# Performance work log

Measured on AMD Instinct MI355X. Metric: run time of the kernel, lower is better.

The kernel has to match this reference:

```python
import jax, jax.numpy as jnp
import numpy as np

T_IN, T_OUT, B, D, H, L = 257, 256, 256, 131, 256, 2


def lstm_cell(x, h, c, Wih, Whh, bih, bhh):
    # torch LSTMCell gate order: i, f, g, o
    z = x @ Wih.T + h @ Whh.T + bih + bhh
    i, f, g, o = jnp.split(z, 4, axis=-1)
    c_new = jax.nn.sigmoid(f) * c + jax.nn.sigmoid(i) * jnp.tanh(g)
    h_new = jax.nn.sigmoid(o) * jnp.tanh(c_new)
    return h_new, c_new


def setup_inputs() -> dict:
    key = jax.random.key(0)
    ks = jax.random.split(key, 22)
    s = 0.05  # weight scale, keeps gates in the linear-ish region
    d = {}
    d["X"] = jax.random.normal(ks[0], (T_IN, B, D), jnp.float32)
    d["Y"] = jax.random.normal(ks[1], (T_OUT, B, D), jnp.float32)
    shapes = {
        "enc_Wih0": (4 * H, D), "enc_Whh0": (4 * H, H), "enc_bih0": (4 * H,), "enc_bhh0": (4 * H,),
        "enc_Wih1": (4 * H, H), "enc_Whh1": (4 * H, H), "enc_bih1": (4 * H,), "enc_bhh1": (4 * H,),
        "dec_Wih0": (4 * H, D), "dec_Whh0": (4 * H, H), "dec_bih0": (4 * H,), "dec_bhh0": (4 * H,),
        "dec_Wih1": (4 * H, H), "dec_Whh1": (4 * H, H), "dec_bih1": (4 * H,), "dec_bhh1": (4 * H,),
        "lin_W": (D, H), "lin_b": (D,),
    }
    for i, (name, shp) in enumerate(shapes.items()):
        d[name] = jax.random.normal(ks[2 + i], shp, jnp.float32) * s
    return d


def _make_step(params, emit):
    def step(carry, x):
        hs, cs = carry
        inp = x
        new_h, new_c = [], []
        for l, (Wih, Whh, bih, bhh) in enumerate(params):
            h, c = lstm_cell(inp, hs[l], cs[l], Wih, Whh, bih, bhh)
            new_h.append(h)
            new_c.append(c)
            inp = h
        out = emit(inp) if emit is not None else None
        return (tuple(new_h), tuple(new_c)), out
    return step


def reference(X, Y, enc_Wih0, enc_Whh0, enc_bih0, enc_bhh0,
              enc_Wih1, enc_Whh1, enc_bih1, enc_bhh1,
              dec_Wih0, dec_Whh0, dec_bih0, dec_bhh0,
              dec_Wih1, dec_Whh1, dec_bih1, dec_bhh1,
              lin_W, lin_b):
    enc = [(enc_Wih0, enc_Whh0, enc_bih0, enc_bhh0),
           (enc_Wih1, enc_Whh1, enc_bih1, enc_bhh1)]
    dec = [(dec_Wih0, dec_Whh0, dec_bih0, dec_bhh0),
           (dec_Wih1, dec_Whh1, dec_bih1, dec_bhh1)]
    b = X.shape[1]
    zeros = tuple(jnp.zeros((b, H), X.dtype) for _ in range(L))
    # encoder over X[:-1]
    (hn, cn), _ = jax.lax.scan(_make_step(enc, None), (zeros, zeros), X[:-1])
    # decoder (teacher forcing): inputs are [X[-1], Y[0], ..., Y[T_out-2]]
    dec_in = jnp.concatenate([X[-1:], Y[:-1]], axis=0)
    emit = lambda h: jax.nn.log_softmax(h @ lin_W.T + lin_b, axis=-1)
    _, Ypred = jax.lax.scan(_make_step(dec, emit), (hn, cn), dec_in)
    return Ypred  # (T_out, B, out_dim) log-probabilities
```

## Files before the change

kernel.cpp:

```cpp
#include <hip/hip_runtime.h>
#include <hip/hip_bf16.h>
#include <math.h>

typedef __attribute__((ext_vector_type(8))) short short8;
typedef __attribute__((ext_vector_type(4))) float f32x4;
typedef unsigned long long u64;

#define STEPS 512
#define BB 256
#define HH 256
#define DD 131
#define XP 160
#define K0P 416
#define KS0 424
#define K1  512
#define KS1 520
#define HS0 264
#define HS1 520
#define RING 16
#define PO   8
#define NGRP 8
#define ROWS 32
#define SLOT_E (ROWS * HH)
#define RGELEM (RING * SLOT_E)
#define POISON64 0x7F807F807F807F80ull

#define OFF_W0E 0
#define OFF_W0D (OFF_W0E + 1024 * K0P)
#define OFF_W1E (OFF_W0D + 1024 * K0P)
#define OFF_W1D (OFF_W1E + 1024 * K1)
#define OFF_LW  (OFF_W1D + 1024 * K1)
#define OFF_XBF (OFF_LW + 160 * 256)
#define OFF_H0R (OFF_XBF + (size_t)STEPS * BB * XP)
#define OFF_H1R (OFF_H0R + (size_t)NGRP * RGELEM)
#define OFF_H1A (OFF_H1R + (size_t)NGRP * RGELEM)
#define OFF_BF16_END (OFF_H1A + (size_t)256 * BB * HH)

#define LDS_W_OFF  0
#define LDS_HS_OFF 66560
#define LDS_TOTAL  133120

__device__ __forceinline__ float rcp_(float x) { return __builtin_amdgcn_rcpf(x); }
__device__ __forceinline__ float fsigm(float x) { return rcp_(1.f + __expf(-x)); }
__device__ __forceinline__ float ftanh(float x) {
    float t = __expf(-2.f * fabsf(x));
    float r = (1.f - t) * rcp_(1.f + t);
    return copysignf(r, x);
}
__device__ __forceinline__ u64 aload(const u64* p) {
    return __hip_atomic_load(p, __ATOMIC_RELAXED, __HIP_MEMORY_SCOPE_AGENT);
}
__device__ __forceinline__ void astore(u64* p, u64 v) {
    __hip_atomic_store(p, v, __ATOMIC_RELAXED, __HIP_MEMORY_SCOPE_AGENT);
}

__global__ __launch_bounds__(256) void pack_w0(const float* __restrict__ Wih,
                                               const float* __restrict__ Whh,
                                               __hip_bfloat16* __restrict__ dst) {
    int idx = blockIdx.x * 256 + threadIdx.x;
    int p = idx / K0P, k = idx - p * K0P;
    int ct = p >> 6, local = p & 63, g = local >> 4, j = local & 15;
    int orow = g * 256 + ct * 16 + j;
    float v = 0.f;
    if (k < DD) v = Wih[orow * DD + k];
    else if (k >= XP) v = Whh[orow * HH + (k - XP)];
    dst[idx] = __float2bfloat16(v);
}

__global__ __launch_bounds__(256) void pack_w1(const float* __restrict__ Wih,
                                               const float* __restrict__ Whh,
                                               __hip_bfloat16* __restrict__ dst) {
    int idx = blockIdx.x * 256 + threadIdx.x;
    int p = idx >> 9, k = idx & 511;
    int ct = p >> 6, local = p & 63, g = local >> 4, j = local & 15;
    int orow = g * 256 + ct * 16 + j;
    float v = (k < HH) ? Wih[orow * HH + k] : Whh[orow * HH + (k - HH)];
    dst[idx] = __float2bfloat16(v);
}

__global__ __launch_bounds__(256) void pack_bias(const float* __restrict__ bih,
                                                 const float* __restrict__ bhh,
                                                 float* __restrict__ dst) {
    int idx = blockIdx.x * 256 + threadIdx.x;
    if (idx < 1024) dst[idx] = bih[idx] + bhh[idx];
}

__global__ __launch_bounds__(256) void pack_xbf(const float* __restrict__ X,
                                                const float* __restrict__ Y,
                                                __hip_bfloat16* __restrict__ dst) {
    int idx = blockIdx.x * 256 + threadIdx.x;
    int kp = idx % XP;
    int rb = idx / XP;
    int b = rb & 255, s = rb >> 8;
    const float* src;
    if (s <= 256) src = X + ((size_t)s * BB + b) * DD;
    else          src = Y + ((size_t)(s - 257) * BB + b) * DD;
    dst[idx] = __float2bfloat16(kp < DD ? src[kp] : 0.f);
}

__global__ __launch_bounds__(256) void pack_linw(const float* __restrict__ linW,
                                                 __hip_bfloat16* __restrict__ dst) {
    int idx = blockIdx.x * 256 + threadIdx.x;
    int j = idx >> 8, k = idx & 255;
    dst[idx] = __float2bfloat16(j < DD ? linW[j * HH + k] : 0.f);
}

__global__ __launch_bounds__(256) void pack_linb(const float* __restrict__ linb,
                                                 float* __restrict__ dst) {
    int idx = threadIdx.x;
    if (idx < 160) dst[idx] = (idx < DD) ? linb[idx] : -1.0e30f;
}

__global__ __launch_bounds__(256) void init_rings(u64* __restrict__ rings,
                                                  int* __restrict__ acks) {
    int idx = blockIdx.x * 256 + threadIdx.x;
    if (idx < 2 * NGRP * (RGELEM / 4)) {
        int slot = (idx >> 11) & (RING - 1);
        rings[idx] = (slot == RING - 1) ? 0ull : POISON64;
    }
    if (idx < 256) acks[idx] = 0;
}

__global__ __launch_bounds__(512, 1) void lstm_persistent(
    const __hip_bfloat16* __restrict__ wsb,
    const float* __restrict__ bsum,
    __hip_bfloat16* __restrict__ h0ring,
    __hip_bfloat16* __restrict__ h1ring,
    __hip_bfloat16* __restrict__ h1all,
    int* __restrict__ acks) {
    extern __shared__ __align__(16) char lds[];
    __hip_bfloat16* Wlds = (__hip_bfloat16*)(lds + LDS_W_OFF);
    __hip_bfloat16* hst  = (__hip_bfloat16*)(lds + LDS_HS_OFF);

    const int tid = threadIdx.x;
    const int wg = blockIdx.x;
    const int xg = wg >> 5;
    const int slot_id = wg & 31;
    const int layer = slot_id >> 4;
    const int ct = slot_id & 15;
    const int lane = tid & 63;
    const int mt = tid >> 6;
    const int lrow = lane & 15;
    const int lk8 = (lane >> 4) * 8;

    const int K  = layer ? K1 : K0P;
    const int KS = layer ? KS1 : KS0;
    const int HS = layer ? HS1 : HS0;
    int* ackp = acks + xg * 32;

    auto load_w = [&](int ph2) {
        const __hip_bfloat16* src = wsb +
            (layer ? (ph2 ? OFF_W1D : OFF_W1E) : (ph2 ? OFF_W0D : OFF_W0E)) +
            (size_t)ct * 64 * K;
        const int KC = K >> 3;
        for (int e = tid; e < 64 * KC; e += 512) {
            int p = e / KC, kc = e - p * KC;
            *(short8*)&Wlds[p * KS + kc * 8] =
                *(const short8*)&src[(size_t)p * K + kc * 8];
        }
    };
    load_w(0);

    const int jcol = ct * 16 + lrow;
    float br[2][4];
    #pragma unroll
    for (int ph = 0; ph < 2; ++ph)
        #pragma unroll
        for (int g = 0; g < 4; ++g)
            br[ph][g] = bsum[ph * 2048 + layer * 1024 + g * 256 + jcol];
    f32x4 creg = {0.f, 0.f, 0.f, 0.f};

    const __hip_bfloat16* Xbf = wsb + OFF_XBF;
    __hip_bfloat16* h0g = h0ring + (size_t)xg * RGELEM;
    __hip_bfloat16* h1g = h1ring + (size_t)xg * RGELEM;
    __hip_bfloat16* ringw = layer ? h1g : h0g;
    const int arow = mt * 16 + lrow;
    __syncthreads();

    for (int s = 0; s < STEPS; ++s) {
        const int ph = s >> 8;
        const bool defer_x = (s == 256);
        f32x4 acc[4];
        short8 xv[5];

        if (tid < 128) {
            #pragma unroll
            for (int g = 0; g < 4; ++g) acc[g] = (f32x4){0.f, 0.f, 0.f, 0.f};
            if (layer == 0) {
                const short8* xp = (const short8*)
                    &Xbf[((size_t)s * BB + xg * ROWS + arow) * XP];
                #pragma unroll
                for (int kt = 0; kt < 5; ++kt) xv[kt] = xp[kt * 4 + (lk8 >> 3)];
                if (!defer_x) {
                    #pragma unroll
                    for (int kt = 0; kt < 5; ++kt)
                        #pragma unroll
                        for (int g = 0; g < 4; ++g) {
                            short8 w = *(const short8*)
                                &Wlds[(g * 16 + lrow) * KS0 + kt * 32 + lk8];
                            acc[g] = __builtin_amdgcn_mfma_f32_16x16x32_bf16(
                                xv[kt], w, acc[g], 0, 0, 0);
                        }
                }
            }
        } else {
            const int ptid = tid - 128;
            __hip_bfloat16* hs = hst + (s & 1) * 32 * HS;
            if (layer == 0) {
                const u64* src = (const u64*)(h0g +
                    (size_t)((s + RING - 1) & (RING - 1)) * SLOT_E);
                u64 v[6];
                unsigned pend = 0;
                #pragma unroll
                for (int i = 0; i < 6; ++i)
                    if (ptid + i * 384 < 2048) pend |= (1u << i);
                int guard = 0;
                while (pend) {
                    #pragma unroll
                    for (int i = 0; i < 6; ++i)
                        if (pend & (1u << i)) v[i] = aload(src + ptid + i * 384);
                    unsigned np = 0;
                    #pragma unroll
                    for (int i = 0; i < 6; ++i)
                        if ((pend & (1u << i)) &&
                            ((v[i] & 0xFFFFull) == 0x7F80ull)) np |= (1u << i);
                    pend = np;
                    if (pend) {
                        __builtin_amdgcn_s_sleep(1);
                        if (++guard > 65536) break;
                    }
                }
                #pragma unroll
                for (int i = 0; i < 6; ++i) {
                    int p = ptid + i * 384;
                    if (p < 2048) {
                        int row = p >> 6, c = p & 63;
                        *(u64*)&hs[row * HS0 + c * 4] = v[i];
                    }
                }
                if (ptid == 383) {
                    int tgt = 16 * (s - (PO - 1));
                    if (tgt > 0) {
                        int guard2 = 0;
                        while (__hip_atomic_load(ackp, __ATOMIC_RELAXED,
                                                 __HIP_MEMORY_SCOPE_AGENT) < tgt) {
                            __builtin_amdgcn_s_sleep(1);
                            if (++guard2 > 65536) break;
                        }
                    }
                }
            } else {
                const u64* s0 = (const u64*)(h0g +
                    (size_t)(s & (RING - 1)) * SLOT_E);
                const u64* s1 = (const u64*)(h1g +
                    (size_t)((s + RING - 1) & (RING - 1)) * SLOT_E);
                u64 v[11];
                unsigned pend = 0;
                #pragma unroll
                for (int i = 0; i < 11; ++i)
                    if (ptid + i * 384 < 4096) pend |= (1u << i);
                int guard = 0;
                while (pend) {
                    #pragma unroll
                    for (int i = 0; i < 11; ++i)
                        if (pend & (1u << i)) {
                            int p = ptid + i * 384;
                            v[i] = aload(p < 2048 ? s0 + p : s1 + (p - 2048));
                        }
                    unsigned np = 0;
                    #pragma unroll
                    for (int i = 0; i < 11; ++i)
                        if ((pend & (1u << i)) &&
                            ((v[i] & 0xFFFFull) == 0x7F80ull)) np |= (1u << i);
                    pend = np;
                    if (pend) {
                        __builtin_amdgcn_s_sleep(1);
                        if (++guard > 65536) break;
                    }
                }
                #pragma unroll
                for (int i = 0; i < 11; ++i) {
                    int p = ptid + i * 384;
                    if (p < 4096) {
                        int pr = p & 2047;
                        int row = pr >> 6, c = pr & 63;
                        *(u64*)&hs[row * HS1 + (p < 2048 ? 0 : 256) + c * 4] = v[i];
                    }
                }
            }
        }
        __syncthreads();
        if (s == 256) { load_w(1); __syncthreads(); }

        if (tid < 128) {
            if (layer == 1 && tid == 0)
                __hip_atomic_fetch_add(ackp, 1, __ATOMIC_RELAXED,
                                       __HIP_MEMORY_SCOPE_AGENT);
            const __hip_bfloat16* hs = hst + (s & 1) * 32 * HS;
            if (layer == 0) {
                if (defer_x) {
                    #pragma unroll
                    for (int kt = 0; kt < 5; ++kt)
                        #pragma unroll
                        for (int g = 0; g < 4; ++g) {
                            short8 w = *(const short8*)
                                &Wlds[(g * 16 + lrow) * KS0 + kt * 32 + lk8];
                            acc[g] = __builtin_amdgcn_mfma_f32_16x16x32_bf16(
                                xv[kt], w, acc[g], 0, 0, 0);
                        }
                }
                #pragma unroll
                for (int kt = 0; kt < 8; ++kt) {
                    short8 a = *(const short8*)&hs[arow * HS0 + kt * 32 + lk8];
                    #pragma unroll
                    for (int g = 0; g < 4; ++g) {
                        short8 w = *(const short8*)
                            &Wlds[(g * 16 + lrow) * KS0 + (5 + kt) * 32 + lk8];
                        acc[g] = __builtin_amdgcn_mfma_f32_16x16x32_bf16(
                            a, w, acc[g], 0, 0, 0);
                    }
                }
            } else {
                #pragma unroll
                for (int kt = 0; kt < 16; ++kt) {
                    short8 a = *(const short8*)&hs[arow * HS1 + kt * 32 + lk8];
                    #pragma unroll
                    for (int g = 0; g < 4; ++g) {
                        short8 w = *(const short8*)
                            &Wlds[(g * 16 + lrow) * KS1 + kt * 32 + lk8];
                        acc[g] = __builtin_amdgcn_mfma_f32_16x16x32_bf16(
                            a, w, acc[g], 0, 0, 0);
                    }
                }
            }

            unsigned short hu[4];
            #pragma unroll
            for (int r = 0; r < 4; ++r) {
                float zi = acc[0][r] + br[ph][0];
                float zf = acc[1][r] + br[ph][1];
                float zg = acc[2][r] + br[ph][2];
                float zo = acc[3][r] + br[ph][3];
                float ig = fsigm(zi), fg = fsigm(zf), og = fsigm(zo);
                float cn = fg * creg[r] + ig * ftanh(zg);
                creg[r] = cn;
                union { __hip_bfloat16 b; unsigned short u; } cvt;
                cvt.b = __float2bfloat16(og * ftanh(cn));
                hu[r] = cvt.u;
            }

            {
                const int m = lane & 15, g16 = lane >> 4;
                const int srcbase = g16 * 16 + 4 * (m & 3);
                const int myslot = m >> 2;
                unsigned short pa = 0, pb = 0, pc = 0, pd = 0;
                #pragma unroll
                for (int rr = 0; rr < 4; ++rr) {
                    int q0 = __shfl((int)hu[rr], srcbase + 0, 64);
                    int q1 = __shfl((int)hu[rr], srcbase + 1, 64);
                    int q2 = __shfl((int)hu[rr], srcbase + 2, 64);
                    int q3 = __shfl((int)hu[rr], srcbase + 3, 64);
                    if (myslot == rr) {
                        pa = (unsigned short)q0; pb = (unsigned short)q1;
                        pc = (unsigned short)q2; pd = (unsigned short)q3;
                    }
                }
                u64 pkt = (u64)pa | ((u64)pb << 16) | ((u64)pc << 32)
                        | ((u64)pd << 48);
                const int prow = mt * 16 + g16 * 4 + myslot;
                const int pq = m & 3;
                astore((u64*)(ringw + (size_t)(s & (RING - 1)) * SLOT_E)
                       + prow * 64 + ct * 4 + pq, pkt);
                if (layer == 1 && s >= 256)
                    *(u64*)&h1all[((size_t)(s - 256) * BB + xg * ROWS + prow) * HH
                                  + ct * 16 + pq * 4] = pkt;
                astore((u64*)(ringw + (size_t)((s + PO) & (RING - 1)) * SLOT_E)
                       + prow * 64 + ct * 4 + pq, POISON64);
            }
        }
    }
}

__global__ __launch_bounds__(256) void emit_mfma(
    const __hip_bfloat16* __restrict__ h1all,
    const __hip_bfloat16* __restrict__ lW,
    const float* __restrict__ lb,
    float* __restrict__ out) {
    __shared__ float lbs[160];
    const int tid = threadIdx.x;
    const int wv = tid >> 6, lane = tid & 63;
    const int lrow = lane & 15, lk8 = (lane >> 4) * 8, crow = (lane >> 4) * 4;
    const int row0 = blockIdx.x * 64;
    if (tid < 160) lbs[tid] = lb[tid];
    __syncthreads();

    f32x4 acc[10];
    #pragma unroll
    for (int f = 0; f < 10; ++f) acc[f] = (f32x4){0.f, 0.f, 0.f, 0.f};
    const int arow = row0 + wv * 16 + lrow;
    #pragma unroll
    for (int kt = 0; kt < 8; ++kt) {
        short8 a = *reinterpret_cast<const short8*>(
            &h1all[(size_t)arow * HH + kt * 32 + lk8]);
        #pragma unroll
        for (int f = 0; f < 10; ++f) {
            short8 w = *reinterpret_cast<const short8*>(
                &lW[(size_t)(f * 16 + lrow) * HH + kt * 32 + lk8]);
            acc[f] = __builtin_amdgcn_mfma_f32_16x16x32_bf16(a, w, acc[f], 0, 0, 0);
        }
    }
    #pragma unroll
    for (int r = 0; r < 4; ++r) {
        float m = -3.0e38f;
        #pragma unroll
        for (int f = 0; f < 10; ++f) m = fmaxf(m, acc[f][r] + lbs[f * 16 + lrow]);
        #pragma unroll
        for (int d = 1; d < 16; d <<= 1) m = fmaxf(m, __shfl_xor(m, d, 64));
        float ss = 0.f;
        #pragma unroll
        for (int f = 0; f < 10; ++f) ss += __expf(acc[f][r] + lbs[f * 16 + lrow] - m);
        #pragma unroll
        for (int d = 1; d < 16; d <<= 1) ss += __shfl_xor(ss, d, 64);
        float lse = m + logf(ss);
        int grow = row0 + wv * 16 + crow + r;
        #pragma unroll
        for (int f = 0; f < 9; ++f) {
            int j = f * 16 + lrow;
            if (j < DD)
                out[(size_t)grow * DD + j] = acc[f][r] + lbs[j] - lse;
        }
    }
}

extern "C" void kernel_launch(void* const* d_in, const int* in_sizes, int n_in,
                              void* d_out, int out_size, void* d_ws, size_t ws_size,
                              hipStream_t stream) {
    const float* X     = (const float*)d_in[0];
    const float* Y     = (const float*)d_in[1];
    const float* eWih0 = (const float*)d_in[2];
    const float* eWhh0 = (const float*)d_in[3];
    const float* ebih0 = (const float*)d_in[4];
    const float* ebhh0 = (const float*)d_in[5];
    const float* eWih1 = (const float*)d_in[6];
    const float* eWhh1 = (const float*)d_in[7];
    const float* ebih1 = (const float*)d_in[8];
    const float* ebhh1 = (const float*)d_in[9];
    const float* dWih0 = (const float*)d_in[10];
    const float* dWhh0 = (const float*)d_in[11];
    const float* dbih0 = (const float*)d_in[12];
    const float* dbhh0 = (const float*)d_in[13];
    const float* dWih1 = (const float*)d_in[14];
    const float* dWhh1 = (const float*)d_in[15];
    const float* dbih1 = (const float*)d_in[16];
    const float* dbhh1 = (const float*)d_in[17];
    const float* linW  = (const float*)d_in[18];
    const float* linb  = (const float*)d_in[19];
    float* out = (float*)d_out;

    __hip_bfloat16* wsb = (__hip_bfloat16*)d_ws;
    float* freg  = (float*)(wsb + OFF_BF16_END);
    float* bsum  = freg;
    float* linbp = freg + 4096;
    int*   acks  = (int*)(freg + 4096 + 192);

    pack_w0<<<dim3(1664), dim3(256), 0, stream>>>(eWih0, eWhh0, wsb + OFF_W0E);
    pack_w0<<<dim3(1664), dim3(256), 0, stream>>>(dWih0, dWhh0, wsb + OFF_W0D);
    pack_w1<<<dim3(2048), dim3(256), 0, stream>>>(eWih1, eWhh1, wsb + OFF_W1E);
    pack_w1<<<dim3(2048), dim3(256), 0, stream>>>(dWih1, dWhh1, wsb + OFF_W1D);
    pack_bias<<<dim3(4), dim3(256), 0, stream>>>(ebih0, ebhh0, bsum + 0);
    pack_bias<<<dim3(4), dim3(256), 0, stream>>>(ebih1, ebhh1, bsum + 1024);
    pack_bias<<<dim3(4), dim3(256), 0, stream>>>(dbih0, dbhh0, bsum + 2048);
    pack_bias<<<dim3(4), dim3(256), 0, stream>>>(dbih1, dbhh1, bsum + 3072);
    pack_xbf<<<dim3(81920), dim3(256), 0, stream>>>(X, Y, wsb + OFF_XBF);
    pack_linw<<<dim3(160), dim3(256), 0, stream>>>(linW, wsb + OFF_LW);
    pack_linb<<<dim3(1), dim3(256), 0, stream>>>(linb, linbp);
    init_rings<<<dim3(2048), dim3(256), 0, stream>>>((u64*)(wsb + OFF_H0R), acks);

    hipFuncSetAttribute((const void*)lstm_persistent,
                        hipFuncAttributeMaxDynamicSharedMemorySize, LDS_TOTAL);
    lstm_persistent<<<dim3(256), dim3(512), LDS_TOTAL, stream>>>(
        wsb, bsum, wsb + OFF_H0R, wsb + OFF_H1R, wsb + OFF_H1A, acks);

    emit_mfma<<<dim3(1024), dim3(256), 0, stream>>>(wsb + OFF_H1A, wsb + OFF_LW,
                                                    linbp, out);
}
```

Before: 2.470 ms.

## Split layer-1 wait so recurrent-state matmul overlaps polling for layer-0 output

Layer-1 blocks used to poll for both their own previous hidden state and the layer-0 output of the current step before running any MFMA. Now they first wait only for their own recurrent half and run the K-half of the matmul on it, while producer threads separately poll for the fresh layer-0 ring slot. The remaining half runs after that arrives. This hides part of the inter-layer pipeline latency behind compute. The cost is an extra __syncthreads per step, and the poison store is moved before the h1all write so the next slot is marked earlier.

```diff
diff --git a/kernel.cpp b/kernel.cpp
--- a/kernel.cpp
+++ b/kernel.cpp
@@ -250,26 +250,21 @@
                     }
                 }
             } else {
-                const u64* s0 = (const u64*)(h0g +
-                    (size_t)(s & (RING - 1)) * SLOT_E);
                 const u64* s1 = (const u64*)(h1g +
                     (size_t)((s + RING - 1) & (RING - 1)) * SLOT_E);
-                u64 v[11];
+                u64 v[6];
                 unsigned pend = 0;
                 #pragma unroll
-                for (int i = 0; i < 11; ++i)
-                    if (ptid + i * 384 < 4096) pend |= (1u << i);
+                for (int i = 0; i < 6; ++i)
+                    if (ptid + i * 384 < 2048) pend |= (1u << i);
                 int guard = 0;
                 while (pend) {
                     #pragma unroll
-                    for (int i = 0; i < 11; ++i)
-                        if (pend & (1u << i)) {
-                            int p = ptid + i * 384;
-                            v[i] = aload(p < 2048 ? s0 + p : s1 + (p - 2048));
-                        }
+                    for (int i = 0; i < 6; ++i)
+                        if (pend & (1u << i)) v[i] = aload(s1 + ptid + i * 384);
                     unsigned np = 0;
                     #pragma unroll
-                    for (int i = 0; i < 11; ++i)
+                    for (int i = 0; i < 6; ++i)
                         if ((pend & (1u << i)) &&
                             ((v[i] & 0xFFFFull) == 0x7F80ull)) np |= (1u << i);
                     pend = np;
@@ -279,13 +274,64 @@
                     }
                 }
                 #pragma unroll
-                for (int i = 0; i < 11; ++i) {
+                for (int i = 0; i < 6; ++i) {
                     int p = ptid + i * 384;
-                    if (p < 4096) {
-                        int pr = p & 2047;
-                        int row = pr >> 6, c = pr & 63;
-                        *(u64*)&hs[row * HS1 + (p < 2048 ? 0 : 256) + c * 4] = v[i];
-                    }
+                    if (p < 2048) {
+                        int row = p >> 6, c = p & 63;
+                        *(u64*)&hs[row * HS1 + 256 + c * 4] = v[i];
+                    }
+                }
+            }
+        }
+        __syncthreads();
+
+        if (tid < 128) {
+            if (layer == 1) {
+                const __hip_bfloat16* hs = hst + (s & 1) * 32 * HS1;
+                #pragma unroll
+                for (int kt = 8; kt < 16; ++kt) {
+                    short8 a = *(const short8*)&hs[arow * HS1 + kt * 32 + lk8];
+                    #pragma unroll
+                    for (int g = 0; g < 4; ++g) {
+                        short8 w = *(const short8*)
+                            &Wlds[(g * 16 + lrow) * KS1 + kt * 32 + lk8];
+                        acc[g] = __builtin_amdgcn_mfma_f32_16x16x32_bf16(
+                            a, w, acc[g], 0, 0, 0);
+                    }
+                }
+            }
+        } else if (layer == 1) {
+            const int ptid = tid - 128;
+            __hip_bfloat16* hs = hst + (s & 1) * 32 * HS1;
+            const u64* s0 = (const u64*)(h0g +
+                (size_t)(s & (RING - 1)) * SLOT_E);
+            u64 v[6];
+            unsigned pend = 0;
+            #pragma unroll
+            for (int i = 0; i < 6; ++i)
+                if (ptid + i * 384 < 2048) pend |= (1u << i);
+            int guard = 0;
+            while (pend) {
+                #pragma unroll
+                for (int i = 0; i < 6; ++i)
+                    if (pend & (1u << i)) v[i] = aload(s0 + ptid + i * 384);
+                unsigned np = 0;
+                #pragma unroll
+                for (int i = 0; i < 6; ++i)
+                    if ((pend & (1u << i)) &&
+                        ((v[i] & 0xFFFFull) == 0x7F80ull)) np |= (1u << i);
+                pend = np;
+                if (pend) {
+                    __builtin_amdgcn_s_sleep(1);
+                    if (++guard > 65536) break;
+                }
+            }
+            #pragma unroll
+            for (int i = 0; i < 6; ++i) {
+                int p = ptid + i * 384;
+                if (p < 2048) {
+                    int row = p >> 6, c = p & 63;
+                    *(u64*)&hs[row * HS1 + c * 4] = v[i];
                 }
             }
         }
@@ -322,7 +368,7 @@
                 }
             } else {
                 #pragma unroll
-                for (int kt = 0; kt < 16; ++kt) {
+                for (int kt = 0; kt < 8; ++kt) {
                     short8 a = *(const short8*)&hs[arow * HS1 + kt * 32 + lk8];
                     #pragma unroll
                     for (int g = 0; g < 4; ++g) {
@@ -371,11 +417,11 @@
                 const int pq = m & 3;
                 astore((u64*)(ringw + (size_t)(s & (RING - 1)) * SLOT_E)
                        + prow * 64 + ct * 4 + pq, pkt);
+                astore((u64*)(ringw + (size_t)((s + PO) & (RING - 1)) * SLOT_E)
+                       + prow * 64 + ct * 4 + pq, POISON64);
                 if (layer == 1 && s >= 256)
                     *(u64*)&h1all[((size_t)(s - 256) * BB + xg * ROWS + prow) * HH
                                   + ct * 16 + pq * 4] = pkt;
-                astore((u64*)(ringw + (size_t)((s + PO) & (RING - 1)) * SLOT_E)
-                       + prow * 64 + ct * 4 + pq, POISON64);
             }
         }
     }
```

Result: slower. 2.740 ms (+11.0%).
